# Kernel optimization log

Measured on AMD Instinct MI355X. Metric: run time of the kernel, lower is better.

Reference implementation:

```python
import jax, jax.numpy as jnp
import numpy as np

LUT_DIM = 33
CTX_DIM = 128


def _identity_lut(dim):
    coords = jnp.linspace(0.0, 1.0, dim)
    r, g, b = jnp.meshgrid(coords, coords, coords, indexing='ij')
    return jnp.stack([r, g, b], axis=-1)  # [dim, dim, dim, 3], axes (r,g,b)


def setup_inputs() -> dict:
    key = jax.random.key(0)
    ks = jax.random.split(key, 8)
    B, H, W = 4, 512, 512
    image = jax.random.normal(ks[0], (B, 3, H, W), dtype=jnp.float32)
    spatial_context = jax.random.normal(ks[1], (B, CTX_DIM, H, W), dtype=jnp.float32)
    s = 0.05
    params = {
        'base_lut': _identity_lut(LUT_DIM),
        'W1': jax.random.normal(ks[2], (128, CTX_DIM), dtype=jnp.float32) * s,
        'b1': jnp.zeros((128,), dtype=jnp.float32),
        'W2': jax.random.normal(ks[3], (64, 128), dtype=jnp.float32) * s,
        'b2': jnp.zeros((64,), dtype=jnp.float32),
        'W3': jax.random.normal(ks[4], (3, 64), dtype=jnp.float32) * s,
        'b3': jnp.zeros((3,), dtype=jnp.float32),
        'offset_scale': jnp.float32(0.1),
    }
    return {'image': image, 'spatial_context': spatial_context, **params}


def _conv1x1(x, W, b):
    # x: [B,Cin,H,W], W: [Cout,Cin]
    return jnp.einsum('bchw,oc->bohw', x, W) + b[None, :, None, None]


def _trilinear_lut(lut_flat, gx, gy, gz, dim):
    # lut_flat: [3, dim^3] (flattened over z,y,x = r,g,b axes)
    # gx,gy,gz: [B,H,W] float coords in [0, dim-1]; border padding via clamp
    fmax = jnp.float32(dim - 1)
    gx = jnp.clip(gx, 0.0, fmax)
    gy = jnp.clip(gy, 0.0, fmax)
    gz = jnp.clip(gz, 0.0, fmax)
    x0 = jnp.floor(gx).astype(jnp.int32)
    y0 = jnp.floor(gy).astype(jnp.int32)
    z0 = jnp.floor(gz).astype(jnp.int32)
    x1 = jnp.minimum(x0 + 1, dim - 1)
    y1 = jnp.minimum(y0 + 1, dim - 1)
    z1 = jnp.minimum(z0 + 1, dim - 1)
    fx = gx - x0.astype(gx.dtype)
    fy = gy - y0.astype(gy.dtype)
    fz = gz - z0.astype(gz.dtype)

    def gather(zi, yi, xi):
        idx = (zi * dim + yi) * dim + xi  # [B,H,W]
        return lut_flat[:, idx]  # [3,B,H,W]

    c000 = gather(z0, y0, x0); c001 = gather(z0, y0, x1)
    c010 = gather(z0, y1, x0); c011 = gather(z0, y1, x1)
    c100 = gather(z1, y0, x0); c101 = gather(z1, y0, x1)
    c110 = gather(z1, y1, x0); c111 = gather(z1, y1, x1)

    fx = fx[None]; fy = fy[None]; fz = fz[None]
    c00 = c000 * (1 - fx) + c001 * fx
    c01 = c010 * (1 - fx) + c011 * fx
    c10 = c100 * (1 - fx) + c101 * fx
    c11 = c110 * (1 - fx) + c111 * fx
    c0 = c00 * (1 - fy) + c01 * fy
    c1 = c10 * (1 - fy) + c11 * fy
    out = c0 * (1 - fz) + c1 * fz  # [3,B,H,W]
    return jnp.transpose(out, (1, 0, 2, 3))  # [B,3,H,W]


def reference(image, spatial_context, base_lut, W1, b1, W2, b2, W3, b3, offset_scale):
    dim = base_lut.shape[0]
    gelu = lambda v: jax.nn.gelu(v, approximate=False)
    h = gelu(_conv1x1(spatial_context, W1, b1))
    h = gelu(_conv1x1(h, W2, b2))
    offset = jnp.tanh(_conv1x1(h, W3, b3)) * offset_scale  # [B,3,H,W]

    img01 = jnp.clip((image + 1.0) * 0.5, 0.0, 1.0)
    # grid_sample convention: grid channel0 (R)->x->last LUT axis (b),
    # channel1 (G)->y->g axis, channel2 (B)->z->r axis; align_corners=True.
    scale = jnp.float32(dim - 1)
    gx = img01[:, 0] * scale  # R -> b axis
    gy = img01[:, 1] * scale  # G -> g axis
    gz = img01[:, 2] * scale  # B -> r axis
    # base_lut [r,g,b,3] -> channels-first [3, r(=z), g(=y), b(=x)] -> flatten
    lut_flat = jnp.transpose(base_lut, (3, 0, 1, 2)).reshape(3, dim * dim * dim)
    sampled = _trilinear_lut(lut_flat, gx, gy, gz, dim)  # [B,3,H,W]
    return sampled * 2.0 - 1.0 + offset
```

## Files before the change

kernel.cpp:

```cpp
#include <hip/hip_runtime.h>
#include <stdint.h>

#define HW 262144
#define LDIM 33

typedef __bf16 bf16x8 __attribute__((ext_vector_type(8)));
typedef __bf16 bf16x2 __attribute__((ext_vector_type(2)));
typedef float  f32x4  __attribute__((ext_vector_type(4)));

union BF8 { bf16x8 v; unsigned u[4]; };

__device__ __forceinline__ unsigned pk2(float a, float b) {
  bf16x2 p; p[0] = (__bf16)a; p[1] = (__bf16)b;
  return __builtin_bit_cast(unsigned, p);
}
__device__ __forceinline__ float exp2_hw(float x) {
  return __builtin_amdgcn_exp2f(x);
}
__device__ __forceinline__ float tanh_fast(float x) {
  float t = exp2_hw(x * 2.8853900818f);
  return 1.0f - __fdividef(2.0f, t + 1.0f);
}
__device__ __forceinline__ float gelu_t(float x) {
  float x2 = x * x;
  float p2 = x * fmaf(0.1029425216f, x2, 2.3021667f);
  float r  = __fdividef(1.0f, exp2_hw(p2) + 1.0f);
  return fmaf(-x, r, x);
}

struct F3 { float x, y, z; };
__device__ __forceinline__ F3 lerp3(F3 a, F3 b, float f) {
  F3 r; r.x = a.x + f * (b.x - a.x); r.y = a.y + f * (b.y - a.y);
  r.z = a.z + f * (b.z - a.z); return r;
}

__global__ __launch_bounds__(512, 4) void mlp_offset_kernel(
    const float* __restrict__ ctx,  const float* __restrict__ W1,
    const float* __restrict__ b1,   const float* __restrict__ W2,
    const float* __restrict__ b2,   const float* __restrict__ W3,
    const float* __restrict__ b3,   const float* __restrict__ oscp,
    float* __restrict__ out)
{
  __shared__ uint4 smem4[4096];
  char* sm = (char*)smem4;
  const int t    = threadIdx.x;
  const int lane = t & 63;
  const int wv   = t >> 6;
  const int n    = lane & 15;
  const int q    = lane >> 4;

  #pragma unroll
  for (int rep = 0; rep < 8; ++rep) {
    int f4 = t + 512 * rep;
    float4 v = ((const float4*)W1)[f4];
    int fi = f4 << 2;
    int o = fi >> 7, k = fi & 127;
    char* dst = sm + o * 256 + (((k >> 3) ^ (o & 15)) << 4) + ((k & 7) << 1);
    *(uint2*)dst = make_uint2(pk2(v.x, v.y), pk2(v.z, v.w));
  }
  #pragma unroll
  for (int rep = 0; rep < 4; ++rep) {
    int f4 = t + 512 * rep;
    float4 v = ((const float4*)W2)[f4];
    int fi = f4 << 2;
    int o = fi >> 7, k = fi & 127;
    char* dst = sm + 32768 + o * 256 + (((k >> 3) ^ (o & 15)) << 4) + ((k & 7) << 1);
    *(uint2*)dst = make_uint2(pk2(v.x, v.y), pk2(v.z, v.w));
  }
  __syncthreads();

  float b1r[8];
  #pragma unroll
  for (int i = 0; i < 8; ++i) b1r[i] = b1[i * 16 + n];
  float b2r[4];
  #pragma unroll
  for (int i = 0; i < 4; ++i) b2r[i] = b2[i * 16 + n];
  BF8 w3a[2];
  #pragma unroll
  for (int ks3 = 0; ks3 < 2; ++ks3) {
    #pragma unroll
    for (int m = 0; m < 4; ++m) {
      float e0 = 0.f, e1 = 0.f;
      if (n < 3) {
        e0 = W3[n * 64 + ks3 * 32 + q * 8 + 2 * m];
        e1 = W3[n * 64 + ks3 * 32 + q * 8 + 2 * m + 1];
      }
      w3a[ks3].u[m] = pk2(e0, e1);
    }
  }
  const float b3a0 = b3[0], b3a1 = b3[1], b3a2 = b3[2];
  const float osc  = oscp[0];

  const int p0   = blockIdx.x * 1024;
  const int bi   = p0 >> 18;
  const int sblk = p0 & (HW - 1);
  const float* ctxB = ctx + (size_t)bi * ((size_t)128 * HW);
  float*       outB = out + (size_t)bi * ((size_t)3 * HW);
  char* hb = sm + 49152 + wv * 2048;

  #pragma unroll 1
  for (int it = 0; it < 8; ++it) {
    const int sw = sblk + it * 128 + wv * 16;

    BF8 a1[4];
    {
      const int sA = sw + n;
      #pragma unroll
      for (int ks = 0; ks < 4; ++ks) {
        const float* cb = ctxB + (size_t)(ks * 32 + q * 8) * HW + sA;
        float v0 = cb[0];
        float v1 = cb[(size_t)1 * HW];
        float v2 = cb[(size_t)2 * HW];
        float v3 = cb[(size_t)3 * HW];
        float v4 = cb[(size_t)4 * HW];
        float v5 = cb[(size_t)5 * HW];
        float v6 = cb[(size_t)6 * HW];
        float v7 = cb[(size_t)7 * HW];
        a1[ks].u[0] = pk2(v0, v1);
        a1[ks].u[1] = pk2(v2, v3);
        a1[ks].u[2] = pk2(v4, v5);
        a1[ks].u[3] = pk2(v6, v7);
      }
    }

    f32x4 acc2[4];
    #pragma unroll
    for (int j = 0; j < 4; ++j) { f32x4 z = {0.f,0.f,0.f,0.f}; acc2[j] = z; }

    #pragma unroll
    for (int half = 0; half < 2; ++half) {
      f32x4 acc1[4];
      #pragma unroll
      for (int j = 0; j < 4; ++j) { f32x4 z = {0.f,0.f,0.f,0.f}; acc1[j] = z; }

      #pragma unroll
      for (int ks = 0; ks < 4; ++ks) {
        #pragma unroll
        for (int nt4 = 0; nt4 < 4; ++nt4) {
          int row = (half * 4 + nt4) * 16 + n;
          bf16x8 bw = *(const bf16x8*)(sm + row * 256 + ((((ks << 2) + q) ^ n) << 4));
          acc1[nt4] = __builtin_amdgcn_mfma_f32_16x16x32_bf16(a1[ks].v, bw, acc1[nt4], 0, 0, 0);
        }
      }
      #pragma unroll
      for (int nt4 = 0; nt4 < 4; ++nt4) {
        int fl = nt4 * 16 + n;
        int kgf = fl >> 3;
        #pragma unroll
        for (int r = 0; r < 4; ++r) {
          int px = (q << 2) + r;
          float hv = gelu_t(acc1[nt4][r] + b1r[half * 4 + nt4]);
          *(__bf16*)(hb + px * 128 + ((kgf ^ (px & 7)) << 4) + ((fl & 7) << 1)) = (__bf16)hv;
        }
      }
      #pragma unroll
      for (int ks2 = 0; ks2 < 2; ++ks2) {
        bf16x8 a2 = *(const bf16x8*)(hb + n * 128 + ((((ks2 << 2) + q) ^ (n & 7)) << 4));
        #pragma unroll
        for (int nt2 = 0; nt2 < 4; ++nt2) {
          int row = nt2 * 16 + n;
          int kg2 = half * 8 + (ks2 << 2) + q;
          bf16x8 bw = *(const bf16x8*)(sm + 32768 + row * 256 + ((kg2 ^ n) << 4));
          acc2[nt2] = __builtin_amdgcn_mfma_f32_16x16x32_bf16(a2, bw, acc2[nt2], 0, 0, 0);
        }
      }
    }

    #pragma unroll
    for (int nt2 = 0; nt2 < 4; ++nt2) {
      int kgW = (nt2 << 1) + (n >> 3);
      #pragma unroll
      for (int r = 0; r < 4; ++r) {
        int px = (q << 2) + r;
        float hv = gelu_t(acc2[nt2][r] + b2r[nt2]);
        *(__bf16*)(hb + px * 128 + ((kgW ^ (px & 7)) << 4) + ((n & 7) << 1)) = (__bf16)hv;
      }
    }

    f32x4 acc3 = {0.f, 0.f, 0.f, 0.f};
    #pragma unroll
    for (int ks3 = 0; ks3 < 2; ++ks3) {
      bf16x8 hf = *(const bf16x8*)(hb + n * 128 + ((((ks3 << 2) + q) ^ (n & 7)) << 4));
      acc3 = __builtin_amdgcn_mfma_f32_16x16x32_bf16(w3a[ks3].v, hf, acc3, 0, 0, 0);
    }
    const int ba = n << 2;
    float d0 = __int_as_float(__builtin_amdgcn_ds_bpermute(ba, __float_as_int(acc3[0])));
    float d1 = __int_as_float(__builtin_amdgcn_ds_bpermute(ba, __float_as_int(acc3[1])));
    float d2 = __int_as_float(__builtin_amdgcn_ds_bpermute(ba, __float_as_int(acc3[2])));

    if (q < 3) {
      float sel  = (q == 0) ? d0   : ((q == 1) ? d1   : d2);
      float bsel = (q == 0) ? b3a0 : ((q == 1) ? b3a1 : b3a2);
      outB[q * HW + sw + n] = tanh_fast(sel + bsel) * osc;
    }
  }
}

__global__ __launch_bounds__(256) void lut_apply_kernel(
    const float* __restrict__ img, const float* __restrict__ lut,
    float* __restrict__ out)
{
  const int p  = blockIdx.x * 256 + threadIdx.x;
  const int b  = p >> 18;
  const int sp = p & (HW - 1);
  const float* imgB = img + (size_t)b * ((size_t)3 * HW);
  float*       outB = out + (size_t)b * ((size_t)3 * HW);

  const float rr = imgB[sp];
  const float gg = imgB[HW + sp];
  const float bb = imgB[2 * HW + sp];
  const float o0 = outB[sp];
  const float o1 = outB[HW + sp];
  const float o2 = outB[2 * HW + sp];

  float gx = fminf(fmaxf(fmaf(rr, 16.f, 16.f), 0.f), 32.f);
  float gy = fminf(fmaxf(fmaf(gg, 16.f, 16.f), 0.f), 32.f);
  float gz = fminf(fmaxf(fmaf(bb, 16.f, 16.f), 0.f), 32.f);
  int x0 = (int)gx, y0 = (int)gy, z0 = (int)gz;
  float fx = gx - (float)x0, fy = gy - (float)y0, fz = gz - (float)z0;
  int x1 = min(x0 + 1, 32), y1 = min(y0 + 1, 32), z1 = min(z0 + 1, 32);
  int zy00 = (z0 * LDIM + y0) * LDIM, zy01 = (z0 * LDIM + y1) * LDIM;
  int zy10 = (z1 * LDIM + y0) * LDIM, zy11 = (z1 * LDIM + y1) * LDIM;
  const F3* L3 = (const F3*)lut;
  F3 c000 = L3[zy00 + x0], c001 = L3[zy00 + x1];
  F3 c010 = L3[zy01 + x0], c011 = L3[zy01 + x1];
  F3 c100 = L3[zy10 + x0], c101 = L3[zy10 + x1];
  F3 c110 = L3[zy11 + x0], c111 = L3[zy11 + x1];
  F3 c00 = lerp3(c000, c001, fx), c01 = lerp3(c010, c011, fx);
  F3 c10 = lerp3(c100, c101, fx), c11 = lerp3(c110, c111, fx);
  F3 ca  = lerp3(c00, c01, fy),   cb2 = lerp3(c10, c11, fy);
  F3 so  = lerp3(ca, cb2, fz);
  outB[sp]          = fmaf(so.x, 2.f, -1.f) + o0;
  outB[HW + sp]     = fmaf(so.y, 2.f, -1.f) + o1;
  outB[2 * HW + sp] = fmaf(so.z, 2.f, -1.f) + o2;
}

extern "C" void kernel_launch(void* const* d_in, const int* in_sizes, int n_in,
                              void* d_out, int out_size, void* d_ws, size_t ws_size,
                              hipStream_t stream) {
  const float* img = (const float*)d_in[0];
  const float* ctx = (const float*)d_in[1];
  const float* lut = (const float*)d_in[2];
  const float* W1  = (const float*)d_in[3];
  const float* b1  = (const float*)d_in[4];
  const float* W2  = (const float*)d_in[5];
  const float* b2  = (const float*)d_in[6];
  const float* W3  = (const float*)d_in[7];
  const float* b3  = (const float*)d_in[8];
  const float* osc = (const float*)d_in[9];
  float* out = (float*)d_out;
  mlp_offset_kernel<<<dim3(1024), dim3(512), 0, stream>>>(
      ctx, W1, b1, W2, b2, W3, b3, osc, out);
  lut_apply_kernel<<<dim3(4096), dim3(256), 0, stream>>>(img, lut, out);
}
```

Before: 794.6 us.

## Prefetch next context tile into registers and process two M-tiles per wave

The MLP kernel now uses 256-thread blocks over 512 pixels. Each wave handles 32 pixels per iteration as two 16-row MFMA tiles that share each LDS weight fragment, so weight reads from LDS are reused twice. The next iteration's context values are loaded into registers while the current tile is computed, a software prefetch meant to hide global-load latency on this memory-bound stage. The cost is much higher VGPR use (raw prefetch buffer plus doubled accumulators), which could reduce occupancy or cause spills, and per-block weight staging is spread over fewer threads.

Measured after the change: 807.7 us. About the same (+1.7%).

```diff
diff --git a/kernel.cpp b/kernel.cpp
--- a/kernel.cpp
+++ b/kernel.cpp
@@ -34,7 +34,22 @@
   r.z = a.z + f * (b.z - a.z); return r;
 }
 
-__global__ __launch_bounds__(512, 4) void mlp_offset_kernel(
+__device__ __forceinline__ void load_raw(float (&raw)[2][4][8],
+    const float* __restrict__ ctxB, int swb, int n, int q) {
+  #pragma unroll
+  for (int mt = 0; mt < 2; ++mt) {
+    const int sA = swb + mt * 16 + n;
+    #pragma unroll
+    for (int ks = 0; ks < 4; ++ks) {
+      const float* cb = ctxB + (size_t)(ks * 32 + q * 8) * HW + sA;
+      #pragma unroll
+      for (int j = 0; j < 8; ++j)
+        raw[mt][ks][j] = cb[(size_t)j * HW];
+    }
+  }
+}
+
+__global__ __launch_bounds__(256, 2) void mlp_offset_kernel(
     const float* __restrict__ ctx,  const float* __restrict__ W1,
     const float* __restrict__ b1,   const float* __restrict__ W2,
     const float* __restrict__ b2,   const float* __restrict__ W3,
@@ -50,8 +65,8 @@
   const int q    = lane >> 4;
 
   #pragma unroll
-  for (int rep = 0; rep < 8; ++rep) {
-    int f4 = t + 512 * rep;
+  for (int rep = 0; rep < 16; ++rep) {
+    int f4 = t + 256 * rep;
     float4 v = ((const float4*)W1)[f4];
     int fi = f4 << 2;
     int o = fi >> 7, k = fi & 127;
@@ -59,8 +74,8 @@
     *(uint2*)dst = make_uint2(pk2(v.x, v.y), pk2(v.z, v.w));
   }
   #pragma unroll
-  for (int rep = 0; rep < 4; ++rep) {
-    int f4 = t + 512 * rep;
+  for (int rep = 0; rep < 8; ++rep) {
+    int f4 = t + 256 * rep;
     float4 v = ((const float4*)W2)[f4];
     int fi = f4 << 2;
     int o = fi >> 7, k = fi & 127;
@@ -91,47 +106,47 @@
   const float b3a0 = b3[0], b3a1 = b3[1], b3a2 = b3[2];
   const float osc  = oscp[0];
 
-  const int p0   = blockIdx.x * 1024;
+  const int p0   = blockIdx.x * 512;
   const int bi   = p0 >> 18;
   const int sblk = p0 & (HW - 1);
   const float* ctxB = ctx + (size_t)bi * ((size_t)128 * HW);
   float*       outB = out + (size_t)bi * ((size_t)3 * HW);
-  char* hb = sm + 49152 + wv * 2048;
-
-  #pragma unroll 1
-  for (int it = 0; it < 8; ++it) {
-    const int sw = sblk + it * 128 + wv * 16;
-
-    BF8 a1[4];
-    {
-      const int sA = sw + n;
+  char* hb = sm + 49152 + wv * 4096;
+
+  float raw[2][4][8];
+  load_raw(raw, ctxB, sblk + wv * 32, n, q);
+
+  #pragma unroll
+  for (int it = 0; it < 4; ++it) {
+    const int sw = sblk + it * 128 + wv * 32;
+
+    BF8 a1[2][4];
+    #pragma unroll
+    for (int mt = 0; mt < 2; ++mt)
       #pragma unroll
       for (int ks = 0; ks < 4; ++ks) {
-        const float* cb = ctxB + (size_t)(ks * 32 + q * 8) * HW + sA;
-        float v0 = cb[0];
-        float v1 = cb[(size_t)1 * HW];
-        float v2 = cb[(size_t)2 * HW];
-        float v3 = cb[(size_t)3 * HW];
-        float v4 = cb[(size_t)4 * HW];
-        float v5 = cb[(size_t)5 * HW];
-        float v6 = cb[(size_t)6 * HW];
-        float v7 = cb[(size_t)7 * HW];
-        a1[ks].u[0] = pk2(v0, v1);
-        a1[ks].u[1] = pk2(v2, v3);
-        a1[ks].u[2] = pk2(v4, v5);
-        a1[ks].u[3] = pk2(v6, v7);
-      }
-    }
-
-    f32x4 acc2[4];
-    #pragma unroll
-    for (int j = 0; j < 4; ++j) { f32x4 z = {0.f,0.f,0.f,0.f}; acc2[j] = z; }
+        a1[mt][ks].u[0] = pk2(raw[mt][ks][0], raw[mt][ks][1]);
+        a1[mt][ks].u[1] = pk2(raw[mt][ks][2], raw[mt][ks][3]);
+        a1[mt][ks].u[2] = pk2(raw[mt][ks][4], raw[mt][ks][5]);
+        a1[mt][ks].u[3] = pk2(raw[mt][ks][6], raw[mt][ks][7]);
+      }
+
+    if (it < 3)
+      load_raw(raw, ctxB, sblk + (it + 1) * 128 + wv * 32, n, q);
+
+    f32x4 acc2[2][4];
+    #pragma unroll
+    for (int mt = 0; mt < 2; ++mt)
+      #pragma unroll
+      for (int j = 0; j < 4; ++j) { f32x4 z = {0.f,0.f,0.f,0.f}; acc2[mt][j] = z; }
 
     #pragma unroll
     for (int half = 0; half < 2; ++half) {
-      f32x4 acc1[4];
-      #pragma unroll
-      for (int j = 0; j < 4; ++j) { f32x4 z = {0.f,0.f,0.f,0.f}; acc1[j] = z; }
+      f32x4 acc1[2][4];
+      #pragma unroll
+      for (int mt = 0; mt < 2; ++mt)
+        #pragma unroll
+        for (int j = 0; j < 4; ++j) { f32x4 z = {0.f,0.f,0.f,0.f}; acc1[mt][j] = z; }
 
       #pragma unroll
       for (int ks = 0; ks < 4; ++ks) {
@@ -139,59 +154,81 @@
         for (int nt4 = 0; nt4 < 4; ++nt4) {
           int row = (half * 4 + nt4) * 16 + n;
           bf16x8 bw = *(const bf16x8*)(sm + row * 256 + ((((ks << 2) + q) ^ n) << 4));
-          acc1[nt4] = __builtin_amdgcn_mfma_f32_16x16x32_bf16(a1[ks].v, bw, acc1[nt4], 0, 0, 0);
-        }
-      }
-      #pragma unroll
-      for (int nt4 = 0; nt4 < 4; ++nt4) {
-        int fl = nt4 * 16 + n;
-        int kgf = fl >> 3;
-        #pragma unroll
-        for (int r = 0; r < 4; ++r) {
-          int px = (q << 2) + r;
-          float hv = gelu_t(acc1[nt4][r] + b1r[half * 4 + nt4]);
-          *(__bf16*)(hb + px * 128 + ((kgf ^ (px & 7)) << 4) + ((fl & 7) << 1)) = (__bf16)hv;
-        }
-      }
+          acc1[0][nt4] = __builtin_amdgcn_mfma_f32_16x16x32_bf16(a1[0][ks].v, bw, acc1[0][nt4], 0, 0, 0);
+          acc1[1][nt4] = __builtin_amdgcn_mfma_f32_16x16x32_bf16(a1[1][ks].v, bw, acc1[1][nt4], 0, 0, 0);
+        }
+      }
+      #pragma unroll
+      for (int mt = 0; mt < 2; ++mt)
+        #pragma unroll
+        for (int nt4 = 0; nt4 < 4; ++nt4) {
+          int fl = nt4 * 16 + n;
+          int kgf = fl >> 3;
+          #pragma unroll
+          for (int r = 0; r < 4; ++r) {
+            int px = mt * 16 + (q << 2) + r;
+            float hv = gelu_t(acc1[mt][nt4][r] + b1r[half * 4 + nt4]);
+            *(__bf16*)(hb + px * 128 + ((kgf ^ (px & 7)) << 4) + ((fl & 7) << 1)) = (__bf16)hv;
+          }
+        }
       #pragma unroll
       for (int ks2 = 0; ks2 < 2; ++ks2) {
-        bf16x8 a2 = *(const bf16x8*)(hb + n * 128 + ((((ks2 << 2) + q) ^ (n & 7)) << 4));
+        bf16x8 a2[2];
+        #pragma unroll
+        for (int mt = 0; mt < 2; ++mt) {
+          int px = mt * 16 + n;
+          a2[mt] = *(const bf16x8*)(hb + px * 128 + ((((ks2 << 2) + q) ^ (px & 7)) << 4));
+        }
         #pragma unroll
         for (int nt2 = 0; nt2 < 4; ++nt2) {
           int row = nt2 * 16 + n;
           int kg2 = half * 8 + (ks2 << 2) + q;
           bf16x8 bw = *(const bf16x8*)(sm + 32768 + row * 256 + ((kg2 ^ n) << 4));
-          acc2[nt2] = __builtin_amdgcn_mfma_f32_16x16x32_bf16(a2, bw, acc2[nt2], 0, 0, 0);
-        }
-      }
-    }
-
-    #pragma unroll
-    for (int nt2 = 0; nt2 < 4; ++nt2) {
-      int kgW = (nt2 << 1) + (n >> 3);
-      #pragma unroll
-      for (int r = 0; r < 4; ++r) {
-        int px = (q << 2) + r;
-        float hv = gelu_t(acc2[nt2][r] + b2r[nt2]);
-        *(__bf16*)(hb + px * 128 + ((kgW ^ (px & 7)) << 4) + ((n & 7) << 1)) = (__bf16)hv;
-      }
-    }
-
-    f32x4 acc3 = {0.f, 0.f, 0.f, 0.f};
-    #pragma unroll
-    for (int ks3 = 0; ks3 < 2; ++ks3) {
-      bf16x8 hf = *(const bf16x8*)(hb + n * 128 + ((((ks3 << 2) + q) ^ (n & 7)) << 4));
-      acc3 = __builtin_amdgcn_mfma_f32_16x16x32_bf16(w3a[ks3].v, hf, acc3, 0, 0, 0);
+          acc2[0][nt2] = __builtin_amdgcn_mfma_f32_16x16x32_bf16(a2[0], bw, acc2[0][nt2], 0, 0, 0);
+          acc2[1][nt2] = __builtin_amdgcn_mfma_f32_16x16x32_bf16(a2[1], bw, acc2[1][nt2], 0, 0, 0);
+        }
+      }
+    }
+
+    #pragma unroll
+    for (int mt = 0; mt < 2; ++mt)
+      #pragma unroll
+      for (int nt2 = 0; nt2 < 4; ++nt2) {
+        int kgW = (nt2 << 1) + (n >> 3);
+        #pragma unroll
+        for (int r = 0; r < 4; ++r) {
+          int px = mt * 16 + (q << 2) + r;
+          float hv = gelu_t(acc2[mt][nt2][r] + b2r[nt2]);
+          *(__bf16*)(hb + px * 128 + ((kgW ^ (px & 7)) << 4) + ((n & 7) << 1)) = (__bf16)hv;
+        }
+      }
+
+    f32x4 acc3[2];
+    #pragma unroll
+    for (int mt = 0; mt < 2; ++mt) {
+      f32x4 z = {0.f, 0.f, 0.f, 0.f};
+      acc3[mt] = z;
+      #pragma unroll
+      for (int ks3 = 0; ks3 < 2; ++ks3) {
+        int px = mt * 16 + n;
+        bf16x8 hf = *(const bf16x8*)(hb + px * 128 + ((((ks3 << 2) + q) ^ (px & 7)) << 4));
+        acc3[mt] = __builtin_amdgcn_mfma_f32_16x16x32_bf16(w3a[ks3].v, hf, acc3[mt], 0, 0, 0);
+      }
     }
     const int ba = n << 2;
-    float d0 = __int_as_float(__builtin_amdgcn_ds_bpermute(ba, __float_as_int(acc3[0])));
-    float d1 = __int_as_float(__builtin_amdgcn_ds_bpermute(ba, __float_as_int(acc3[1])));
-    float d2 = __int_as_float(__builtin_amdgcn_ds_bpermute(ba, __float_as_int(acc3[2])));
+    float d00 = __int_as_float(__builtin_amdgcn_ds_bpermute(ba, __float_as_int(acc3[0][0])));
+    float d01 = __int_as_float(__builtin_amdgcn_ds_bpermute(ba, __float_as_int(acc3[0][1])));
+    float d02 = __int_as_float(__builtin_amdgcn_ds_bpermute(ba, __float_as_int(acc3[0][2])));
+    float d10 = __int_as_float(__builtin_amdgcn_ds_bpermute(ba, __float_as_int(acc3[1][0])));
+    float d11 = __int_as_float(__builtin_amdgcn_ds_bpermute(ba, __float_as_int(acc3[1][1])));
+    float d12 = __int_as_float(__builtin_amdgcn_ds_bpermute(ba, __float_as_int(acc3[1][2])));
 
     if (q < 3) {
-      float sel  = (q == 0) ? d0   : ((q == 1) ? d1   : d2);
+      float sel0 = (q == 0) ? d00 : ((q == 1) ? d01 : d02);
+      float sel1 = (q == 0) ? d10 : ((q == 1) ? d11 : d12);
       float bsel = (q == 0) ? b3a0 : ((q == 1) ? b3a1 : b3a2);
-      outB[q * HW + sw + n] = tanh_fast(sel + bsel) * osc;
+      outB[q * HW + sw + n]      = tanh_fast(sel0 + bsel) * osc;
+      outB[q * HW + sw + 16 + n] = tanh_fast(sel1 + bsel) * osc;
     }
   }
 }
@@ -249,7 +286,7 @@
   const float* b3  = (const float*)d_in[8];
   const float* osc = (const float*)d_in[9];
   float* out = (float*)d_out;
-  mlp_offset_kernel<<<dim3(1024), dim3(512), 0, stream>>>(
+  mlp_offset_kernel<<<dim3(2048), dim3(256), 0, stream>>>(
       ctx, W1, b1, W2, b2, W3, b3, osc, out);
   lut_apply_kernel<<<dim3(4096), dim3(256), 0, stream>>>(img, lut, out);
 }
```
